# Performance work log

Measured on AMD Instinct MI355X. Metric: run time of the kernel, lower is better.

The kernel has to match this reference:

```python
import jax, jax.numpy as jnp
import numpy as np

HIDDEN = 300
INPUT_DIM = 300


def setup_inputs() -> dict:
    key = jax.random.key(0)
    k_in, k_wih, k_whh, k_bih, k_bhh = jax.random.split(key, 5)
    bound = 1.0 / np.sqrt(HIDDEN)  # PyTorch RNNCell init: U(-1/sqrt(H), 1/sqrt(H))
    inputs = jax.random.normal(k_in, (512, 512, INPUT_DIM), dtype=jnp.float32)
    W_ih = jax.random.uniform(k_wih, (HIDDEN, INPUT_DIM), jnp.float32, -bound, bound)
    W_hh = jax.random.uniform(k_whh, (HIDDEN, HIDDEN), jnp.float32, -bound, bound)
    b_ih = jax.random.uniform(k_bih, (HIDDEN,), jnp.float32, -bound, bound)
    b_hh = jax.random.uniform(k_bhh, (HIDDEN,), jnp.float32, -bound, bound)
    return {"inputs": inputs, "W_ih": W_ih, "W_hh": W_hh, "b_ih": b_ih, "b_hh": b_hh}


def reference(inputs, W_ih, W_hh, b_ih, b_hh):
    # inputs: [seq, batch, input_dim]; vanilla tanh RNNCell scanned over time.
    seq, bz, _ = inputs.shape
    # Precompute input projections for all timesteps in one big GEMM.
    x_proj = jnp.einsum('sbi,hi->sbh', inputs, W_ih) + b_ih + b_hh  # [seq, batch, H]

    def step(ht, xp):
        ht = jnp.tanh(xp + ht @ W_hh.T)
        return ht, None

    h0 = jnp.zeros((bz, HIDDEN), dtype=inputs.dtype)
    ht, _ = jax.lax.scan(step, h0, x_proj)
    return ht
```

## Files before the change

### kernel.cpp

```cpp
#include <hip/hip_runtime.h>
#include <hip/hip_bf16.h>


typedef unsigned short u16;
typedef unsigned int   u32;
typedef __attribute__((ext_vector_type(8)))  short bf16x8;
typedef __attribute__((ext_vector_type(4)))  short s16x4;
typedef __attribute__((ext_vector_type(4)))  float f32x4;
typedef __attribute__((ext_vector_type(16))) float f32x16;
typedef __attribute__((ext_vector_type(2)))  unsigned int u32x2;
typedef __attribute__((ext_vector_type(4)))  unsigned int u32x4;

#define HID 300
#define KP  320
#define SEQ 512
#define BZ  512
#define MTOT (SEQ*BZ)

__device__ __forceinline__ u16 f2bf(float f) {
    u32 u = __float_as_uint(f);
    return (u16)((u + 0x7FFFu + ((u >> 16) & 1u)) >> 16);
}
__device__ __forceinline__ float bf2f(u16 h) {
    return __uint_as_float((u32)h << 16);
}
__device__ __forceinline__ float tanh_fast(float x) {
    float e = __builtin_amdgcn_exp2f(x * 2.8853900817779268f);
    float r = __builtin_amdgcn_rcpf(e + 1.0f);
    return __builtin_fmaf(-2.0f, r, 1.0f);
}
__device__ __forceinline__ u32 pack2(float a, float b) {
    __hip_bfloat162 t = __float22bfloat162_rn(float2{a, b});
    return *(u32*)&t;
}
__device__ __forceinline__ void lds_barrier() {
    asm volatile("s_waitcnt lgkmcnt(0)\n\ts_barrier" ::: "memory");
}

__global__ void prep_kernel(const float* __restrict__ wih,
                            const float* __restrict__ whh,
                            const float* __restrict__ bih,
                            const float* __restrict__ bhh,
                            u16* __restrict__ wihp, u16* __restrict__ whhp,
                            float* __restrict__ bias) {
    int n = blockIdx.x, k = threadIdx.x;
    bool v = (n < HID) && (k < HID);
    int src = n * HID + k, dst = n * KP + k;
    wihp[dst] = v ? f2bf(wih[src]) : (u16)0;
    whhp[dst] = v ? f2bf(whh[src]) : (u16)0;
    if (k == 0) bias[n] = (n < HID) ? (bih[n] + bhh[n]) : 0.0f;
}

__global__ __launch_bounds__(512, 1) void xproj_kernel(
    const float* __restrict__ in, const u16* __restrict__ wihp,
    const float* __restrict__ bias, u16* __restrict__ xp) {
    __shared__ __align__(16) u16 As[2][4096];
    __shared__ __align__(16) u16 Bs[3][10240];

    const int tid = threadIdx.x;
    const int w = tid >> 6, l = tid & 63;
    const int mi = w & 3, ni = w >> 2;
    const int l31 = l & 31, l5 = l >> 5;
    const int m0 = blockIdx.x * 128;

    const int sm = tid >> 2, skg = tid & 3;

    f32x16 acc[5];
#pragma unroll
    for (int j = 0; j < 5; ++j)
#pragma unroll
        for (int r = 0; r < 16; ++r) acc[j][r] = 0.0f;

    const f32x4 zf = {0.f, 0.f, 0.f, 0.f};
    auto loadA = [&](int it, f32x4& v0, f32x4& v1) {
        int gk = it * 32 + skg * 8;
        int a0 = gk > 296 ? 296 : gk;
        int a1 = (gk + 4) > 296 ? 296 : (gk + 4);
        const float* p = in + (size_t)(m0 + sm) * HID;
        v0 = *(const f32x4*)(p + a0);
        v1 = *(const f32x4*)(p + a1);
        v0 = (gk > 296) ? zf : v0;
        v1 = ((gk + 4) > 296) ? zf : v1;
    };
    auto writeA = [&](int buf, const f32x4& v0, const f32x4& v1) {
        u32x4 pk;
        pk[0] = pack2(v0[0], v0[1]); pk[1] = pack2(v0[2], v0[3]);
        pk[2] = pack2(v1[0], v1[1]); pk[3] = pack2(v1[2], v1[3]);
        *(u32x4*)&As[buf][(skg >> 1) * 2048 + sm * 16 + (skg & 1) * 8] = pk;
    };
    auto stageB = [&](int buf, int it) {
#pragma unroll
        for (int s = 0; s < 3; ++s) {
            int i = w + 8 * s;
            if (i < 20) {
                int c = i & 3, ng = i >> 2;
                int n = ng * 64 + l;
                const u16* g = wihp + n * KP + it * 32 + c * 8;
                u16* d = &Bs[buf][c * 2560 + ng * 512];
                __builtin_amdgcn_global_load_lds(
                    (const __attribute__((address_space(1))) void*)g,
                    (__attribute__((address_space(3))) void*)d, 16, 0, 0);
            }
        }
    };

    {
        stageB(0, 0);
        f32x4 v0, v1;
        loadA(0, v0, v1);
        writeA(0, v0, v1);
        stageB(1, 1);
        asm volatile("s_waitcnt vmcnt(2)" ::: "memory");
        lds_barrier();
    }

    int cA = 0, cB = 0, sB = 2;
#pragma unroll 1
    for (int it = 0; it < 10; ++it) {
        f32x4 v0, v1;
        if (it < 9) loadA(it + 1, v0, v1);
        if (it < 8) stageB(sB, it + 2);
#pragma unroll
        for (int s = 0; s < 2; ++s) {
            bf16x8 a = *(const bf16x8*)&As[cA][s * 2048 + mi * 512 + l31 * 16 + l5 * 8];
#pragma unroll
            for (int j = 0; j < 5; ++j) {
                bf16x8 b = *(const bf16x8*)&Bs[cB][(s * 2 + l5) * 2560 + ((ni * 5 + j) * 32 + l31) * 8];
                acc[j] = __builtin_amdgcn_mfma_f32_32x32x16_bf16(a, b, acc[j], 0, 0, 0);
            }
        }
        if (it < 9) {
            writeA(cA ^ 1, v0, v1);
            if (it < 8) asm volatile("s_waitcnt vmcnt(3)" ::: "memory");
            else        asm volatile("s_waitcnt vmcnt(2)" ::: "memory");
            lds_barrier();
        }
        cA ^= 1;
        cB = (cB == 2) ? 0 : cB + 1;
        sB = (sB == 2) ? 0 : sB + 1;
    }

    const int mbase = m0 + mi * 32;
#pragma unroll
    for (int j = 0; j < 5; ++j) {
        int n = (ni * 5 + j) * 32 + l31;
        if (n < HID) {
            float bs = bias[n];
#pragma unroll
            for (int reg = 0; reg < 16; ++reg) {
                int row = (reg & 3) + 8 * (reg >> 2) + 4 * l5;
                xp[(size_t)(mbase + row) * HID + n] = f2bf(acc[j][reg] + bs);
            }
        }
    }
}

__global__ __launch_bounds__(512, 2) void rnn_recur_kernel(
    const u16* __restrict__ xp, const u16* __restrict__ whhp,
    float* __restrict__ out, int t0, int t1) {
    __shared__ __align__(16) u16 hb[2][16 * 328];

    const int tid = threadIdx.x;
    const int w = tid >> 6;
    const int l = tid & 63;
    const int br = l & 15;
    const int q  = l >> 4;
    const int b0 = blockIdx.x * 16;
    const bool t3 = (w < 4);

    for (int i = tid; i < (2 * 16 * 328) / 2; i += 512) ((u32*)hb)[i] = 0;

    bf16x8 Af[3][10];
#pragma unroll
    for (int j = 0; j < 3; ++j) {
        if (j < 2 || t3) {
            const int nt = w + 8 * j;
            const u16* wrow = whhp + (size_t)(nt * 16 + br) * KP;
#pragma unroll
            for (int ks = 0; ks < 10; ++ks)
                Af[j][ks] = *(const bf16x8*)(wrow + ks * 32 + q * 8);
        }
    }
#pragma unroll
    for (int j = 0; j < 3; ++j)
        if (j < 2 || t3)
#pragma unroll
            for (int ks = 0; ks < 10; ++ks)
                asm volatile("" : "+a"(Af[j][ks]));

    lds_barrier();
    if (t0 > 0) {
        const u16* hs = (const u16*)out;
        for (int i = tid; i < 16 * HID; i += 512) {
            int r = i / HID, n = i - r * HID;
            hb[0][r * 328 + n] = hs[(size_t)(b0 + r) * HID + n];
        }
    }

    int xo[3];
#pragma unroll
    for (int j = 0; j < 3; ++j) {
        int n0 = (w + 8 * j) * 16 + q * 4;
        xo[j] = (n0 < HID && (j < 2 || t3)) ? ((b0 + br) * HID + n0) : -1;
    }

    const s16x4 z4 = {0, 0, 0, 0};
    s16x4 xc[3], xn[3];
#pragma unroll
    for (int j = 0; j < 3; ++j) {
        xc[j] = (xo[j] >= 0) ? *(const s16x4*)(xp + (size_t)t0 * (BZ * HID) + xo[j]) : z4;
        xn[j] = (xo[j] >= 0) ? *(const s16x4*)(xp + (size_t)(t0 + 1) * (BZ * HID) + xo[j]) : z4;
    }

    lds_barrier();

#pragma unroll 1
    for (int t = t0; t < t1; ++t) {
        const u16* hc = hb[t & 1];
        u16*       hn = hb[(t + 1) & 1];

        s16x4 xf[3];
        {
            int t2 = (t + 2 < SEQ) ? (t + 2) : (SEQ - 1);
            const u16* base = xp + (size_t)t2 * (BZ * HID);
#pragma unroll
            for (int j = 0; j < 3; ++j)
                xf[j] = (xo[j] >= 0) ? *(const s16x4*)(base + xo[j]) : z4;
        }

        f32x4 a0, a1, a2;
#pragma unroll
        for (int r = 0; r < 4; ++r) { a0[r] = 0.f; a1[r] = 0.f; a2[r] = 0.f; }

#pragma unroll
        for (int ks = 0; ks < 10; ++ks) {
            bf16x8 bfr = *(const bf16x8*)&hc[br * 328 + ks * 32 + q * 8];
            a0 = __builtin_amdgcn_mfma_f32_16x16x32_bf16(Af[0][ks], bfr, a0, 0, 0, 0);
            a1 = __builtin_amdgcn_mfma_f32_16x16x32_bf16(Af[1][ks], bfr, a1, 0, 0, 0);
            if (t3)
                a2 = __builtin_amdgcn_mfma_f32_16x16x32_bf16(Af[2][ks], bfr, a2, 0, 0, 0);
        }

        {
            int n0 = w * 16 + q * 4;
            u32x2 pk;
            pk[0] = pack2(tanh_fast(a0[0] + bf2f((u16)xc[0][0])),
                          tanh_fast(a0[1] + bf2f((u16)xc[0][1])));
            pk[1] = pack2(tanh_fast(a0[2] + bf2f((u16)xc[0][2])),
                          tanh_fast(a0[3] + bf2f((u16)xc[0][3])));
            *(u32x2*)&hn[br * 328 + n0] = pk;
        }
        {
            int n0 = (w + 8) * 16 + q * 4;
            u32x2 pk;
            pk[0] = pack2(tanh_fast(a1[0] + bf2f((u16)xc[1][0])),
                          tanh_fast(a1[1] + bf2f((u16)xc[1][1])));
            pk[1] = pack2(tanh_fast(a1[2] + bf2f((u16)xc[1][2])),
                          tanh_fast(a1[3] + bf2f((u16)xc[1][3])));
            *(u32x2*)&hn[br * 328 + n0] = pk;
        }
        if (t3) {
            int n0 = (w + 16) * 16 + q * 4;
            u32x2 pk;
            pk[0] = pack2(tanh_fast(a2[0] + bf2f((u16)xc[2][0])),
                          tanh_fast(a2[1] + bf2f((u16)xc[2][1])));
            pk[1] = pack2(tanh_fast(a2[2] + bf2f((u16)xc[2][2])),
                          tanh_fast(a2[3] + bf2f((u16)xc[2][3])));
            *(u32x2*)&hn[br * 328 + n0] = pk;
        }
        lds_barrier();

#pragma unroll
        for (int j = 0; j < 3; ++j) { xc[j] = xn[j]; xn[j] = xf[j]; }
    }

    const u16* hf = hb[0];
    if (t1 == SEQ) {
        for (int i = tid; i < 16 * HID; i += 512) {
            int r = i / HID, n = i - r * HID;
            out[(size_t)(b0 + r) * HID + n] = bf2f(hf[r * 328 + n]);
        }
    } else {
        u16* hs = (u16*)out;
        for (int i = tid; i < 16 * HID; i += 512) {
            int r = i / HID, n = i - r * HID;
            hs[(size_t)(b0 + r) * HID + n] = hf[r * 328 + n];
        }
    }
}

extern "C" void kernel_launch(void* const* d_in, const int* in_sizes, int n_in,
                              void* d_out, int out_size, void* d_ws, size_t ws_size,
                              hipStream_t stream) {
    const float* in  = (const float*)d_in[0];
    const float* wih = (const float*)d_in[1];
    const float* whh = (const float*)d_in[2];
    const float* bih = (const float*)d_in[3];
    const float* bhh = (const float*)d_in[4];

    char* ws = (char*)d_ws;
    const size_t XP_BYTES = (size_t)MTOT * HID * sizeof(u16);
    u16*   xpb  = (u16*)ws;
    u16*   wihp = (u16*)(ws + XP_BYTES);
    u16*   whhp = (u16*)(ws + XP_BYTES + (size_t)KP * KP * 2);
    float* bias = (float*)(ws + XP_BYTES + 2 * (size_t)KP * KP * 2);

    prep_kernel<<<KP, KP, 0, stream>>>(wih, whh, bih, bhh, wihp, whhp, bias);
    xproj_kernel<<<MTOT / 128, 512, 0, stream>>>(in, wihp, bias, xpb);
    rnn_recur_kernel<<<BZ / 16, 512, 0, stream>>>(xpb, whhp, (float*)d_out, 0, SEQ / 2);
    rnn_recur_kernel<<<BZ / 16, 512, 0, stream>>>(xpb, whhp, (float*)d_out, SEQ / 2, SEQ);
}
```

Before: 1.093 ms.

## Halve batch rows per recurrence block and merge the two time-split launches

The recurrence kernel now handles 8 batch rows per workgroup instead of 16, launching 64 workgroups instead of 32 so more compute units share the serial time loop. The 16-wide MFMA B operand is zero-padded for the unused rows, so half the matrix-core work is wasted. The two launches that split the sequence in half, along with the bf16 hidden-state handoff through the output buffer, are replaced by a single launch covering all 512 steps. This removes one kernel boundary and the save and restore of the hidden state, while each block's per-step latency stays about the same.

Result: slower. 1.124 ms (+2.8%).

```diff
diff --git a/kernel.cpp b/kernel.cpp
--- a/kernel.cpp
+++ b/kernel.cpp
@@ -157,7 +157,7 @@
 
 __global__ __launch_bounds__(512, 2) void rnn_recur_kernel(
     const u16* __restrict__ xp, const u16* __restrict__ whhp,
-    float* __restrict__ out, int t0, int t1) {
+    float* __restrict__ out) {
     __shared__ __align__(16) u16 hb[2][16 * 328];
 
     const int tid = threadIdx.x;
@@ -165,8 +165,9 @@
     const int l = tid & 63;
     const int br = l & 15;
     const int q  = l >> 4;
-    const int b0 = blockIdx.x * 16;
+    const int b0 = blockIdx.x * 8;
     const bool t3 = (w < 4);
+    const bool bv = (br < 8);
 
     for (int i = tid; i < (2 * 16 * 328) / 2; i += 512) ((u32*)hb)[i] = 0;
 
@@ -188,34 +189,25 @@
             for (int ks = 0; ks < 10; ++ks)
                 asm volatile("" : "+a"(Af[j][ks]));
 
-    lds_barrier();
-    if (t0 > 0) {
-        const u16* hs = (const u16*)out;
-        for (int i = tid; i < 16 * HID; i += 512) {
-            int r = i / HID, n = i - r * HID;
-            hb[0][r * 328 + n] = hs[(size_t)(b0 + r) * HID + n];
-        }
-    }
-
     int xo[3];
 #pragma unroll
     for (int j = 0; j < 3; ++j) {
         int n0 = (w + 8 * j) * 16 + q * 4;
-        xo[j] = (n0 < HID && (j < 2 || t3)) ? ((b0 + br) * HID + n0) : -1;
+        xo[j] = (n0 < HID && (j < 2 || t3) && bv) ? ((b0 + br) * HID + n0) : -1;
     }
 
     const s16x4 z4 = {0, 0, 0, 0};
     s16x4 xc[3], xn[3];
 #pragma unroll
     for (int j = 0; j < 3; ++j) {
-        xc[j] = (xo[j] >= 0) ? *(const s16x4*)(xp + (size_t)t0 * (BZ * HID) + xo[j]) : z4;
-        xn[j] = (xo[j] >= 0) ? *(const s16x4*)(xp + (size_t)(t0 + 1) * (BZ * HID) + xo[j]) : z4;
+        xc[j] = (xo[j] >= 0) ? *(const s16x4*)(xp + xo[j]) : z4;
+        xn[j] = (xo[j] >= 0) ? *(const s16x4*)(xp + (size_t)BZ * HID + xo[j]) : z4;
     }
 
     lds_barrier();
 
 #pragma unroll 1
-    for (int t = t0; t < t1; ++t) {
+    for (int t = 0; t < SEQ; ++t) {
         const u16* hc = hb[t & 1];
         u16*       hn = hb[(t + 1) & 1];
 
@@ -234,7 +226,8 @@
 
 #pragma unroll
         for (int ks = 0; ks < 10; ++ks) {
-            bf16x8 bfr = *(const bf16x8*)&hc[br * 328 + ks * 32 + q * 8];
+            bf16x8 bfr = {0, 0, 0, 0, 0, 0, 0, 0};
+            if (bv) bfr = *(const bf16x8*)&hc[br * 328 + ks * 32 + q * 8];
             a0 = __builtin_amdgcn_mfma_f32_16x16x32_bf16(Af[0][ks], bfr, a0, 0, 0, 0);
             a1 = __builtin_amdgcn_mfma_f32_16x16x32_bf16(Af[1][ks], bfr, a1, 0, 0, 0);
             if (t3)
@@ -248,7 +241,7 @@
                           tanh_fast(a0[1] + bf2f((u16)xc[0][1])));
             pk[1] = pack2(tanh_fast(a0[2] + bf2f((u16)xc[0][2])),
                           tanh_fast(a0[3] + bf2f((u16)xc[0][3])));
-            *(u32x2*)&hn[br * 328 + n0] = pk;
+            if (bv) *(u32x2*)&hn[br * 328 + n0] = pk;
         }
         {
             int n0 = (w + 8) * 16 + q * 4;
@@ -257,7 +250,7 @@
                           tanh_fast(a1[1] + bf2f((u16)xc[1][1])));
             pk[1] = pack2(tanh_fast(a1[2] + bf2f((u16)xc[1][2])),
                           tanh_fast(a1[3] + bf2f((u16)xc[1][3])));
-            *(u32x2*)&hn[br * 328 + n0] = pk;
+            if (bv) *(u32x2*)&hn[br * 328 + n0] = pk;
         }
         if (t3) {
             int n0 = (w + 16) * 16 + q * 4;
@@ -266,7 +259,7 @@
                           tanh_fast(a2[1] + bf2f((u16)xc[2][1])));
             pk[1] = pack2(tanh_fast(a2[2] + bf2f((u16)xc[2][2])),
                           tanh_fast(a2[3] + bf2f((u16)xc[2][3])));
-            *(u32x2*)&hn[br * 328 + n0] = pk;
+            if (bv) *(u32x2*)&hn[br * 328 + n0] = pk;
         }
         lds_barrier();
 
@@ -275,17 +268,9 @@
     }
 
     const u16* hf = hb[0];
-    if (t1 == SEQ) {
-        for (int i = tid; i < 16 * HID; i += 512) {
-            int r = i / HID, n = i - r * HID;
-            out[(size_t)(b0 + r) * HID + n] = bf2f(hf[r * 328 + n]);
-        }
-    } else {
-        u16* hs = (u16*)out;
-        for (int i = tid; i < 16 * HID; i += 512) {
-            int r = i / HID, n = i - r * HID;
-            hs[(size_t)(b0 + r) * HID + n] = hf[r * 328 + n];
-        }
+    for (int i = tid; i < 8 * HID; i += 512) {
+        int r = i / HID, n = i - r * HID;
+        out[(size_t)(b0 + r) * HID + n] = bf2f(hf[r * 328 + n]);
     }
 }
 
@@ -307,6 +292,5 @@
 
     prep_kernel<<<KP, KP, 0, stream>>>(wih, whh, bih, bhh, wihp, whhp, bias);
     xproj_kernel<<<MTOT / 128, 512, 0, stream>>>(in, wihp, bias, xpb);
-    rnn_recur_kernel<<<BZ / 16, 512, 0, stream>>>(xpb, whhp, (float*)d_out, 0, SEQ / 2);
-    rnn_recur_kernel<<<BZ / 16, 512, 0, stream>>>(xpb, whhp, (float*)d_out, SEQ / 2, SEQ);
-}
+    rnn_recur_kernel<<<BZ / 8, 512, 0, stream>>>(xpb, whhp, (float*)d_out);
+}
```
